# Kernel optimization log

Measured on AMD Instinct MI355X. Metric: run time of the kernel, lower is better.

Reference implementation:

```python
import jax, jax.numpy as jnp
import numpy as np

N = 100000        # num nodes
E = 1200000       # num edges (avg degree 12)
F_IN = 64         # num_features
HID = 64          # hidden_size
NCLS = 40         # num_classes
K = 2             # propagation hops


def setup_inputs() -> dict:
    key = jax.random.key(0)
    k0, k1, k2, k3 = jax.random.split(key, 4)
    x = jax.random.normal(k0, (N, F_IN), dtype=jnp.float32)
    edge_index = jax.random.randint(k1, (2, E), 0, N, dtype=jnp.int32)
    # SGConv's internal Linear (in->hidden) and the classifier fc (hidden->classes)
    W1 = jax.random.normal(k2, (F_IN, HID), dtype=jnp.float32) / np.sqrt(F_IN).astype(np.float32)
    b1 = jnp.zeros((HID,), jnp.float32)
    W2 = jax.random.normal(k3, (HID, NCLS), dtype=jnp.float32) / np.sqrt(HID).astype(np.float32)
    b2 = jnp.zeros((NCLS,), jnp.float32)
    return {"x": x, "edge_index": edge_index, "W1": W1, "b1": b1, "W2": W2, "b2": b2}


def reference(x, edge_index, W1, b1, W2, b2):
    n = x.shape[0]
    # gcn_norm: add self-loops with weight 1, symmetric normalization
    loop = jnp.arange(n, dtype=edge_index.dtype)
    src = jnp.concatenate([edge_index[0], loop])  # message source j
    dst = jnp.concatenate([edge_index[1], loop])  # aggregation target i
    deg = jax.ops.segment_sum(jnp.ones(src.shape, x.dtype), dst, num_segments=n)
    dinv = jnp.where(deg > 0, jax.lax.rsqrt(deg), 0.0)
    norm = dinv[src] * dinv[dst]  # [E+N]
    # K-hop propagation: x_i <- sum_j norm_ij * x_j
    for _ in range(K):
        x = jax.ops.segment_sum(norm[:, None] * x[src], dst, num_segments=n)
    h = jax.nn.relu(x @ W1 + b1)          # SGConv lin + ReLU
    logits = h @ W2 + b2                  # fc
    return jax.nn.log_softmax(logits, axis=1)
```

## Files before the change

kernel.cpp:

```cpp
#include <hip/hip_runtime.h>
#include <math.h>

#define N_NODES 100000
#define BSHIFT 9
#define NBUCK 256

typedef unsigned short bfu;
typedef unsigned int uint;
typedef __attribute__((ext_vector_type(8))) short short8v;
typedef __attribute__((ext_vector_type(4))) float f32x4;

__device__ __forceinline__ float bf2f(bfu u) {
    union { uint i; float f; } v; v.i = (uint)u << 16; return v.f;
}
__device__ __forceinline__ bfu f2bf(float f) {
    union { float f_; uint i; } v; v.f_ = f;
    uint r = (v.i + 0x7FFFu + ((v.i >> 16) & 1u)) >> 16;
    return (bfu)r;
}

__global__ __launch_bounds__(256) void bucket_hist(const int* __restrict__ dst,
                                                   int* __restrict__ gcount, int nE) {
    __shared__ int h[NBUCK];
    int tid = threadIdx.x;
    h[tid] = 0;
    __syncthreads();
    for (int e = blockIdx.x * 256 + tid; e < nE; e += gridDim.x * 256)
        atomicAdd(&h[dst[e] >> BSHIFT], 1);
    __syncthreads();
    if (h[tid]) atomicAdd(&gcount[tid], h[tid]);
}

__global__ __launch_bounds__(NBUCK) void scan_buckets(const int* __restrict__ gcount,
                                                      int* __restrict__ gbase,
                                                      int* __restrict__ gcursor) {
    __shared__ int s[NBUCK];
    int t = threadIdx.x;
    int v = gcount[t];
    s[t] = v;
    __syncthreads();
    #pragma unroll
    for (int off = 1; off < NBUCK; off <<= 1) {
        int tv = (t >= off) ? s[t - off] : 0;
        __syncthreads();
        s[t] += tv;
        __syncthreads();
    }
    gbase[t] = s[t] - v;
    gcursor[t] = s[t] - v;
}

__global__ __launch_bounds__(256) void bin_edges(const int* __restrict__ src,
                                                 const int* __restrict__ dst,
                                                 int* __restrict__ gcursor,
                                                 uint* __restrict__ binned, int nE) {
    __shared__ int h[NBUCK];
    __shared__ int base[NBUCK];
    int tid = threadIdx.x;
    int start = blockIdx.x * 4096;
    h[tid] = 0;
    __syncthreads();
    int bkt[16], rnk[16];
    #pragma unroll
    for (int u = 0; u < 16; ++u) {
        int e = start + u * 256 + tid;
        bkt[u] = -1;
        if (e < nE) {
            int b = dst[e] >> BSHIFT;
            bkt[u] = b;
            rnk[u] = atomicAdd(&h[b], 1);
        }
    }
    __syncthreads();
    base[tid] = h[tid] ? atomicAdd(&gcursor[tid], h[tid]) : 0;
    __syncthreads();
    #pragma unroll
    for (int u = 0; u < 16; ++u) {
        int e = start + u * 256 + tid;
        if (e < nE) {
            uint pk = ((uint)(dst[e] & 511) << 17) | (uint)src[e];
            binned[base[bkt[u]] + rnk[u]] = pk;
        }
    }
}

__global__ __launch_bounds__(512) void build_csr(
    const uint* __restrict__ binned, const int* __restrict__ gbase,
    const int* __restrict__ gcount, int* __restrict__ rowptr,
    float* __restrict__ dinv, int* __restrict__ nbr,
    const float4* __restrict__ x, ushort4* __restrict__ z0, int nN, int nE) {
    __shared__ int hist[512];
    __shared__ int cursor[512];
    int b = blockIdx.x, t = threadIdx.x;
    int n0 = b << BSHIFT;
    int nNodes = min(512, nN - n0);
    int base = gbase[b], cnt = gcount[b];
    hist[t] = 0;
    __syncthreads();
    for (int i = t; i < cnt; i += 512)
        atomicAdd(&hist[binned[base + i] >> 17], 1);
    __syncthreads();
    int v = hist[t];
    #pragma unroll
    for (int off = 1; off < 512; off <<= 1) {
        int tv = (t >= off) ? hist[t - off] : 0;
        __syncthreads();
        hist[t] += tv;
        __syncthreads();
    }
    int excl = hist[t] - v;
    float dv = rsqrtf((float)v + 1.0f);
    if (t < nNodes) {
        rowptr[n0 + t] = base + excl;
        dinv[n0 + t] = dv;
    }
    cursor[t] = excl;
    ((float*)hist)[t] = dv;
    __syncthreads();
    for (int i = t; i < cnt; i += 512) {
        uint pk = binned[base + i];
        int ld = pk >> 17;
        int pos = atomicAdd(&cursor[ld], 1);
        nbr[base + pos] = (int)(pk & 0x1FFFFu);
    }
    const float4* xr = x + (size_t)n0 * 16;
    ushort4* zr = z0 + (size_t)n0 * 16;
    int totalF4 = nNodes * 16;
    for (int i = t; i < totalF4; i += 512) {
        float w = ((float*)hist)[i >> 4];
        float4 vv = xr[i];
        ushort4 o;
        o.x = f2bf(w * vv.x); o.y = f2bf(w * vv.y);
        o.z = f2bf(w * vv.z); o.w = f2bf(w * vv.w);
        zr[i] = o;
    }
    if (b == 0 && t == 0) rowptr[nN] = nE;
}

template<int PW>
__global__ __launch_bounds__(256, 8) void gather_hop8(
    bfu* __restrict__ out, const bfu* __restrict__ z,
    const int* __restrict__ nbr, const int* __restrict__ rowptr,
    const float* __restrict__ dinv, int nN) {
    int node = blockIdx.x * 4 + (threadIdx.x >> 6);
    if (node >= nN) return;
    int lane = threadIdx.x & 63;
    int g = lane >> 3, k = lane & 7;
    int beg = rowptr[node], end = rowptr[node + 1];

    float acc[8];
    #pragma unroll
    for (int i = 0; i < 8; ++i) acc[i] = 0.f;

    auto rowload = [&](int s) -> uint4 {
        return reinterpret_cast<const uint4*>(z + (size_t)s * 64)[k];
    };
    auto accum = [&](uint4 v) {
        union { uint u; float f; } t;
        t.u = v.x << 16;         acc[0] += t.f;
        t.u = v.x & 0xFFFF0000u; acc[1] += t.f;
        t.u = v.y << 16;         acc[2] += t.f;
        t.u = v.y & 0xFFFF0000u; acc[3] += t.f;
        t.u = v.z << 16;         acc[4] += t.f;
        t.u = v.z & 0xFFFF0000u; acc[5] += t.f;
        t.u = v.w << 16;         acc[6] += t.f;
        t.u = v.w & 0xFFFF0000u; acc[7] += t.f;
    };

    if (g == 0)
        accum(rowload(node));
    int j = beg + g;
    for (; j + 8 < end; j += 16) {
        int i0 = nbr[j], i1 = nbr[j + 8];
        uint4 v0 = rowload(i0);
        uint4 v1 = rowload(i1);
        accum(v0);
        accum(v1);
    }
    if (j < end)
        accum(rowload(nbr[j]));

    #pragma unroll
    for (int m = 8; m < 64; m <<= 1)
        #pragma unroll
        for (int i = 0; i < 8; ++i)
            acc[i] += __shfl_xor(acc[i], m);

    if (g == 0) {
        float di = dinv[node];
        float w = (PW == 2) ? di * di : di;
        uint4 o;
        o.x = ((uint)f2bf(acc[1] * w) << 16) | f2bf(acc[0] * w);
        o.y = ((uint)f2bf(acc[3] * w) << 16) | f2bf(acc[2] * w);
        o.z = ((uint)f2bf(acc[5] * w) << 16) | f2bf(acc[4] * w);
        o.w = ((uint)f2bf(acc[7] * w) << 16) | f2bf(acc[6] * w);
        reinterpret_cast<uint4*>(out + (size_t)node * 64)[k] = o;
    }
}

__global__ __launch_bounds__(256) void mlp_mfma(
    float* __restrict__ out, const bfu* __restrict__ zC,
    const float* __restrict__ W1, const float* __restrict__ b1,
    const float* __restrict__ W2, const float* __restrict__ b2, int nN) {
    __shared__ short w1t[64 * 72];
    __shared__ short w2t[48 * 72];
    __shared__ short hlds[64 * 72];
    __shared__ float b1s[64];
    __shared__ float b2s[48];

    int tid = threadIdx.x;
    for (int i = tid; i < 64 * 64; i += 256) {
        int k = i >> 6, n = i & 63;
        w1t[n * 72 + k] = (short)f2bf(W1[i]);
    }
    for (int i = tid; i < 48 * 64; i += 256) {
        int k = i / 48, n = i % 48;
        w2t[n * 72 + k] = (short)(n < 40 ? f2bf(W2[k * 40 + n]) : 0);
    }
    if (tid < 64) b1s[tid] = b1[tid];
    if (tid >= 64 && tid < 112) b2s[tid - 64] = (tid - 64 < 40) ? b2[tid - 64] : 0.f;

    int wv = tid >> 6, l = tid & 63;
    int li = l & 15, kg = l >> 4;
    int nodebase = blockIdx.x * 64 + wv * 16;
    int nclamp = min(nodebase + li, nN - 1);

    const short8v* zr = (const short8v*)(zC + (size_t)nclamp * 64);
    short8v a0 = zr[kg];
    short8v a1 = zr[kg + 4];
    __syncthreads();

    f32x4 acc[4];
    #pragma unroll
    for (int nt = 0; nt < 4; ++nt) {
        f32x4 c = {0.f, 0.f, 0.f, 0.f};
        short8v b0 = *(const short8v*)&w1t[(nt * 16 + li) * 72 + kg * 8];
        short8v b1f = *(const short8v*)&w1t[(nt * 16 + li) * 72 + 32 + kg * 8];
        c = __builtin_amdgcn_mfma_f32_16x16x32_bf16(a0, b0, c, 0, 0, 0);
        c = __builtin_amdgcn_mfma_f32_16x16x32_bf16(a1, b1f, c, 0, 0, 0);
        acc[nt] = c;
    }
    #pragma unroll
    for (int nt = 0; nt < 4; ++nt) {
        float bb = b1s[nt * 16 + li];
        #pragma unroll
        for (int r = 0; r < 4; ++r) {
            float v = fmaxf(acc[nt][r] + bb, 0.f);
            hlds[(wv * 16 + kg * 4 + r) * 72 + nt * 16 + li] = (short)f2bf(v);
        }
    }
    __syncthreads();

    const short8v* hp = (const short8v*)&hlds[(wv * 16 + li) * 72];
    short8v ha0 = hp[kg];
    short8v ha1 = hp[kg + 4];
    f32x4 acc2[3];
    #pragma unroll
    for (int nt = 0; nt < 3; ++nt) {
        f32x4 c = {0.f, 0.f, 0.f, 0.f};
        short8v b0 = *(const short8v*)&w2t[(nt * 16 + li) * 72 + kg * 8];
        short8v b1f = *(const short8v*)&w2t[(nt * 16 + li) * 72 + 32 + kg * 8];
        c = __builtin_amdgcn_mfma_f32_16x16x32_bf16(ha0, b0, c, 0, 0, 0);
        c = __builtin_amdgcn_mfma_f32_16x16x32_bf16(ha1, b1f, c, 0, 0, 0);
        acc2[nt] = c;
    }

    float lg[3][4];
    #pragma unroll
    for (int nt = 0; nt < 3; ++nt) {
        float bb = b2s[nt * 16 + li];
        #pragma unroll
        for (int r = 0; r < 4; ++r) lg[nt][r] = acc2[nt][r] + bb;
    }
    bool v2 = (li < 8);
    float mx[4], sm[4];
    #pragma unroll
    for (int r = 0; r < 4; ++r) {
        float m = fmaxf(lg[0][r], lg[1][r]);
        if (v2) m = fmaxf(m, lg[2][r]);
        mx[r] = m;
    }
    #pragma unroll
    for (int off = 1; off < 16; off <<= 1)
        #pragma unroll
        for (int r = 0; r < 4; ++r)
            mx[r] = fmaxf(mx[r], __shfl_xor(mx[r], off));
    #pragma unroll
    for (int r = 0; r < 4; ++r) {
        float s = expf(lg[0][r] - mx[r]) + expf(lg[1][r] - mx[r]);
        if (v2) s += expf(lg[2][r] - mx[r]);
        sm[r] = s;
    }
    #pragma unroll
    for (int off = 1; off < 16; off <<= 1)
        #pragma unroll
        for (int r = 0; r < 4; ++r)
            sm[r] += __shfl_xor(sm[r], off);

    int nb2 = nodebase + kg * 4;
    #pragma unroll
    for (int r = 0; r < 4; ++r) {
        int nd = nb2 + r;
        if (nd < nN) {
            float lse = mx[r] + logf(sm[r]);
            out[(size_t)nd * 40 + li]      = lg[0][r] - lse;
            out[(size_t)nd * 40 + 16 + li] = lg[1][r] - lse;
            if (v2) out[(size_t)nd * 40 + 32 + li] = lg[2][r] - lse;
        }
    }
}

extern "C" void kernel_launch(void* const* d_in, const int* in_sizes, int n_in,
                              void* d_out, int out_size, void* d_ws, size_t ws_size,
                              hipStream_t stream) {
    const float* x   = (const float*)d_in[0];
    const int* eidx  = (const int*)d_in[1];
    const float* W1  = (const float*)d_in[2];
    const float* b1  = (const float*)d_in[3];
    const float* W2  = (const float*)d_in[4];
    const float* b2  = (const float*)d_in[5];
    float* out = (float*)d_out;

    const int nN = N_NODES;
    const int nE = in_sizes[1] / 2;
    const int* src = eidx;
    const int* dst = eidx + nE;
    const int nBk = (nN + 511) >> BSHIFT;

    char* ws = (char*)d_ws;
    size_t off = 0;
    auto alloc = [&](size_t bytes) {
        char* p = ws + off;
        off += (bytes + 255) & ~(size_t)255;
        return p;
    };
    float* dinv    = (float*)alloc((size_t)nN * 4);
    int*   gcount  = (int*)  alloc(NBUCK * 4);
    int*   gbase   = (int*)  alloc(NBUCK * 4);
    int*   gcursor = (int*)  alloc(NBUCK * 4);
    int*   rowptr  = (int*)  alloc((size_t)(nN + 1) * 4);
    uint*  binned  = (uint*) alloc((size_t)nE * 4);
    int*   nbr     = (int*)  alloc((size_t)nE * 4);
    bfu*   z0      = (bfu*)  alloc((size_t)nN * 64 * 2);
    bfu*   zB      = (bfu*)  alloc((size_t)nN * 64 * 2);
    bfu*   zC      = (bfu*)  alloc((size_t)nN * 64 * 2);

    hipMemsetAsync(gcount, 0, NBUCK * 4, stream);
    bucket_hist<<<640, 256, 0, stream>>>(dst, gcount, nE);
    scan_buckets<<<1, NBUCK, 0, stream>>>(gcount, gbase, gcursor);
    bin_edges<<<(nE + 4095) / 4096, 256, 0, stream>>>(src, dst, gcursor, binned, nE);
    build_csr<<<nBk, 512, 0, stream>>>(binned, gbase, gcount, rowptr, dinv, nbr,
                                       (const float4*)x, (ushort4*)z0, nN, nE);

    const int gBlocks = (nN + 3) / 4;
    gather_hop8<2><<<gBlocks, 256, 0, stream>>>(zB, z0, nbr, rowptr, dinv, nN);
    gather_hop8<1><<<gBlocks, 256, 0, stream>>>(zC, zB, nbr, rowptr, dinv, nN);

    mlp_mfma<<<(nN + 63) / 64, 256, 0, stream>>>(out, zC, W1, b1, W2, b2, nN);
}
```

Before: 162.2 us.

## Fuse CSR construction stages into one cooperative kernel with grid syncs

Merges the memset, bucket histogram, bucket scan, edge binning and per-bucket CSR build into a single cooperative kernel of nBk blocks (196) of 512 threads. Grid-wide syncs replace the separate launches, and every block recomputes the bucket scan locally so the gbase array is no longer needed. This removes several kernel launch gaps. In exchange, the histogram and binning phases now run on only 196 blocks instead of 640 and 293, so less parallelism is available for those atomic-heavy passes, and the grid syncs add their own cost.

```diff
diff --git a/kernel.cpp b/kernel.cpp
--- a/kernel.cpp
+++ b/kernel.cpp
@@ -1,5 +1,8 @@
 #include <hip/hip_runtime.h>
+#include <hip/hip_cooperative_groups.h>
 #include <math.h>
+
+namespace cg = cooperative_groups;
 
 #define N_NODES 100000
 #define BSHIFT 9
@@ -19,122 +22,127 @@
     return (bfu)r;
 }
 
-__global__ __launch_bounds__(256) void bucket_hist(const int* __restrict__ dst,
-                                                   int* __restrict__ gcount, int nE) {
+__global__ __launch_bounds__(512) void csr_build_all(
+    const int* __restrict__ src, const int* __restrict__ dst,
+    int* __restrict__ gcount, int* __restrict__ gcursor,
+    int* __restrict__ rowptr, float* __restrict__ dinv, int* __restrict__ nbr,
+    const float4* __restrict__ x, ushort4* __restrict__ z0,
+    uint* __restrict__ binned, int nN, int nE) {
+    cg::grid_group grid = cg::this_grid();
     __shared__ int h[NBUCK];
+    __shared__ int sc[NBUCK];
+    __shared__ int lbase[NBUCK];
+    __shared__ int base2[NBUCK];
+    __shared__ int hist2[512];
+    __shared__ int cur2[512];
     int tid = threadIdx.x;
-    h[tid] = 0;
+    int b = blockIdx.x;
+    int nB = gridDim.x;
+
+    for (int i = b * 512 + tid; i < NBUCK; i += nB * 512) gcount[i] = 0;
+    grid.sync();
+
+    if (tid < NBUCK) h[tid] = 0;
     __syncthreads();
-    for (int e = blockIdx.x * 256 + tid; e < nE; e += gridDim.x * 256)
+    for (int e = b * 512 + tid; e < nE; e += nB * 512)
         atomicAdd(&h[dst[e] >> BSHIFT], 1);
     __syncthreads();
-    if (h[tid]) atomicAdd(&gcount[tid], h[tid]);
-}
-
-__global__ __launch_bounds__(NBUCK) void scan_buckets(const int* __restrict__ gcount,
-                                                      int* __restrict__ gbase,
-                                                      int* __restrict__ gcursor) {
-    __shared__ int s[NBUCK];
-    int t = threadIdx.x;
-    int v = gcount[t];
-    s[t] = v;
-    __syncthreads();
-    #pragma unroll
-    for (int off = 1; off < NBUCK; off <<= 1) {
-        int tv = (t >= off) ? s[t - off] : 0;
-        __syncthreads();
-        s[t] += tv;
-        __syncthreads();
-    }
-    gbase[t] = s[t] - v;
-    gcursor[t] = s[t] - v;
-}
-
-__global__ __launch_bounds__(256) void bin_edges(const int* __restrict__ src,
-                                                 const int* __restrict__ dst,
-                                                 int* __restrict__ gcursor,
-                                                 uint* __restrict__ binned, int nE) {
-    __shared__ int h[NBUCK];
-    __shared__ int base[NBUCK];
-    int tid = threadIdx.x;
-    int start = blockIdx.x * 4096;
-    h[tid] = 0;
-    __syncthreads();
-    int bkt[16], rnk[16];
-    #pragma unroll
-    for (int u = 0; u < 16; ++u) {
-        int e = start + u * 256 + tid;
-        bkt[u] = -1;
-        if (e < nE) {
-            int b = dst[e] >> BSHIFT;
-            bkt[u] = b;
-            rnk[u] = atomicAdd(&h[b], 1);
-        }
-    }
-    __syncthreads();
-    base[tid] = h[tid] ? atomicAdd(&gcursor[tid], h[tid]) : 0;
-    __syncthreads();
-    #pragma unroll
-    for (int u = 0; u < 16; ++u) {
-        int e = start + u * 256 + tid;
-        if (e < nE) {
-            uint pk = ((uint)(dst[e] & 511) << 17) | (uint)src[e];
-            binned[base[bkt[u]] + rnk[u]] = pk;
-        }
-    }
-}
-
-__global__ __launch_bounds__(512) void build_csr(
-    const uint* __restrict__ binned, const int* __restrict__ gbase,
-    const int* __restrict__ gcount, int* __restrict__ rowptr,
-    float* __restrict__ dinv, int* __restrict__ nbr,
-    const float4* __restrict__ x, ushort4* __restrict__ z0, int nN, int nE) {
-    __shared__ int hist[512];
-    __shared__ int cursor[512];
-    int b = blockIdx.x, t = threadIdx.x;
-    int n0 = b << BSHIFT;
-    int nNodes = min(512, nN - n0);
-    int base = gbase[b], cnt = gcount[b];
-    hist[t] = 0;
-    __syncthreads();
-    for (int i = t; i < cnt; i += 512)
-        atomicAdd(&hist[binned[base + i] >> 17], 1);
-    __syncthreads();
-    int v = hist[t];
-    #pragma unroll
-    for (int off = 1; off < 512; off <<= 1) {
-        int tv = (t >= off) ? hist[t - off] : 0;
-        __syncthreads();
-        hist[t] += tv;
-        __syncthreads();
-    }
-    int excl = hist[t] - v;
-    float dv = rsqrtf((float)v + 1.0f);
-    if (t < nNodes) {
-        rowptr[n0 + t] = base + excl;
-        dinv[n0 + t] = dv;
-    }
-    cursor[t] = excl;
-    ((float*)hist)[t] = dv;
-    __syncthreads();
-    for (int i = t; i < cnt; i += 512) {
-        uint pk = binned[base + i];
-        int ld = pk >> 17;
-        int pos = atomicAdd(&cursor[ld], 1);
-        nbr[base + pos] = (int)(pk & 0x1FFFFu);
-    }
-    const float4* xr = x + (size_t)n0 * 16;
-    ushort4* zr = z0 + (size_t)n0 * 16;
-    int totalF4 = nNodes * 16;
-    for (int i = t; i < totalF4; i += 512) {
-        float w = ((float*)hist)[i >> 4];
-        float4 vv = xr[i];
-        ushort4 o;
-        o.x = f2bf(w * vv.x); o.y = f2bf(w * vv.y);
-        o.z = f2bf(w * vv.z); o.w = f2bf(w * vv.w);
-        zr[i] = o;
-    }
-    if (b == 0 && t == 0) rowptr[nN] = nE;
+    if (tid < NBUCK && h[tid]) atomicAdd(&gcount[tid], h[tid]);
+    grid.sync();
+
+    {
+        int v = (tid < NBUCK) ? gcount[tid] : 0;
+        if (tid < NBUCK) sc[tid] = v;
+        __syncthreads();
+        #pragma unroll
+        for (int off = 1; off < NBUCK; off <<= 1) {
+            int t2 = (tid >= off && tid < NBUCK) ? sc[tid - off] : 0;
+            __syncthreads();
+            if (tid < NBUCK) sc[tid] += t2;
+            __syncthreads();
+        }
+        if (tid < NBUCK) lbase[tid] = sc[tid] - v;
+        if (b == 0 && tid < NBUCK) gcursor[tid] = sc[tid] - v;
+    }
+    grid.sync();
+
+    for (int chunk = b; (size_t)chunk * 4096 < (size_t)nE; chunk += nB) {
+        int start = chunk * 4096;
+        if (tid < NBUCK) h[tid] = 0;
+        __syncthreads();
+        int bkt[8], rnk[8];
+        #pragma unroll
+        for (int u = 0; u < 8; ++u) {
+            int e = start + u * 512 + tid;
+            bkt[u] = -1;
+            if (e < nE) {
+                int bb = dst[e] >> BSHIFT;
+                bkt[u] = bb;
+                rnk[u] = atomicAdd(&h[bb], 1);
+            }
+        }
+        __syncthreads();
+        if (tid < NBUCK) base2[tid] = h[tid] ? atomicAdd(&gcursor[tid], h[tid]) : 0;
+        __syncthreads();
+        #pragma unroll
+        for (int u = 0; u < 8; ++u) {
+            int e = start + u * 512 + tid;
+            if (e < nE) {
+                uint pk = ((uint)(dst[e] & 511) << 17) | (uint)src[e];
+                binned[base2[bkt[u]] + rnk[u]] = pk;
+            }
+        }
+        __syncthreads();
+    }
+    grid.sync();
+
+    {
+        int n0 = b << BSHIFT;
+        int nNodes = min(512, nN - n0);
+        int base = lbase[b];
+        int cnt = ((b + 1 < NBUCK) ? lbase[b + 1] : nE) - base;
+        hist2[tid] = 0;
+        __syncthreads();
+        for (int i = tid; i < cnt; i += 512)
+            atomicAdd(&hist2[binned[base + i] >> 17], 1);
+        __syncthreads();
+        int v = hist2[tid];
+        #pragma unroll
+        for (int off = 1; off < 512; off <<= 1) {
+            int tv = (tid >= off) ? hist2[tid - off] : 0;
+            __syncthreads();
+            hist2[tid] += tv;
+            __syncthreads();
+        }
+        int excl = hist2[tid] - v;
+        float dv = rsqrtf((float)v + 1.0f);
+        if (tid < nNodes) {
+            rowptr[n0 + tid] = base + excl;
+            dinv[n0 + tid] = dv;
+        }
+        cur2[tid] = excl;
+        __syncthreads();
+        ((float*)hist2)[tid] = dv;
+        __syncthreads();
+        for (int i = tid; i < cnt; i += 512) {
+            uint pk = binned[base + i];
+            int ld = pk >> 17;
+            int pos = atomicAdd(&cur2[ld], 1);
+            nbr[base + pos] = (int)(pk & 0x1FFFFu);
+        }
+        const float4* xr = x + (size_t)n0 * 16;
+        ushort4* zr = z0 + (size_t)n0 * 16;
+        int totalF4 = nNodes * 16;
+        for (int i = tid; i < totalF4; i += 512) {
+            float w = ((float*)hist2)[i >> 4];
+            float4 vv = xr[i];
+            ushort4 o;
+            o.x = f2bf(w * vv.x); o.y = f2bf(w * vv.y);
+            o.z = f2bf(w * vv.z); o.w = f2bf(w * vv.w);
+            zr[i] = o;
+        }
+        if (b == 0 && tid == 0) rowptr[nN] = nE;
+    }
 }
 
 template<int PW>
@@ -336,7 +344,6 @@
     };
     float* dinv    = (float*)alloc((size_t)nN * 4);
     int*   gcount  = (int*)  alloc(NBUCK * 4);
-    int*   gbase   = (int*)  alloc(NBUCK * 4);
     int*   gcursor = (int*)  alloc(NBUCK * 4);
     int*   rowptr  = (int*)  alloc((size_t)(nN + 1) * 4);
     uint*  binned  = (uint*) alloc((size_t)nE * 4);
@@ -345,12 +352,17 @@
     bfu*   zB      = (bfu*)  alloc((size_t)nN * 64 * 2);
     bfu*   zC      = (bfu*)  alloc((size_t)nN * 64 * 2);
 
-    hipMemsetAsync(gcount, 0, NBUCK * 4, stream);
-    bucket_hist<<<640, 256, 0, stream>>>(dst, gcount, nE);
-    scan_buckets<<<1, NBUCK, 0, stream>>>(gcount, gbase, gcursor);
-    bin_edges<<<(nE + 4095) / 4096, 256, 0, stream>>>(src, dst, gcursor, binned, nE);
-    build_csr<<<nBk, 512, 0, stream>>>(binned, gbase, gcount, rowptr, dinv, nbr,
-                                       (const float4*)x, (ushort4*)z0, nN, nE);
+    {
+        int nN_ = nN, nE_ = nE;
+        const float4* x4 = (const float4*)x;
+        ushort4* z04 = (ushort4*)z0;
+        void* args[] = {(void*)&src, (void*)&dst, (void*)&gcount, (void*)&gcursor,
+                        (void*)&rowptr, (void*)&dinv, (void*)&nbr,
+                        (void*)&x4, (void*)&z04, (void*)&binned,
+                        (void*)&nN_, (void*)&nE_};
+        hipLaunchCooperativeKernel((void*)csr_build_all, dim3(nBk), dim3(512),
+                                   args, 0, stream);
+    }
 
     const int gBlocks = (nN + 3) / 4;
     gather_hop8<2><<<gBlocks, 256, 0, stream>>>(zB, z0, nbr, rowptr, dinv, nN);
```

Measured after the change: 239.0 us. +47.4%, slower.
